# Performance work log

Measured on AMD Instinct MI355X. Metric: run time of the kernel, lower is better.

Reference implementation:

```python
import jax, jax.numpy as jnp
import numpy as np
import math

N = 8192
F_IN = 1024
F_OUT = 1024
MAX_ITER = 10


def whale_optimizer(positions, key, max_iter=MAX_ITER):
    """Vectorized whale optimization algorithm.

    Faithful to the original per-agent/per-dim update rules, but the agent
    loop is vectorized (on-device RNG, one parallel update per outer
    iteration); only the `max_iter` outer iterations stay sequential.
    positions: [N, D] float32.
    """
    n, d = positions.shape
    lower = jnp.min(positions)
    upper = jnp.max(positions)
    k0, loop_key = jax.random.split(key)
    leader = positions[jax.random.randint(k0, (), 0, n)]  # [D]

    def step(carry, it):
        pos, leader = carry
        itf = it.astype(jnp.float32)
        k = jax.random.fold_in(loop_key, it)
        k1, k2, k3, k4, k5, k6 = jax.random.split(k, 6)
        a = 2.0 - itf * (2.0 / max_iter)
        a2 = -1.0 + itf * (-1.0 / max_iter)
        r1 = jax.random.uniform(k1, (n, 1))
        r2 = jax.random.uniform(k2, (n, 1))
        A = 2.0 * a * r1 - a                       # [n,1]
        C = 2.0 * r2                               # [n,1]
        lp = (a2 - 1.0) * jax.random.uniform(k3, (n, 1)) + 1.0  # spiral param
        p = jax.random.uniform(k4, (n, 1))
        # random leader per (agent, dim), as in the original inner j-loop
        ridx = jax.random.randint(k5, (n, d), 0, n)
        x_rand = jnp.take_along_axis(pos, ridx, axis=0)         # [n,d]
        explore = jnp.abs(x_rand - A * jnp.abs(C * x_rand - pos))
        exploit = jnp.abs(leader - A * jnp.abs(C * leader - pos))
        spiral = jnp.abs(jnp.abs(leader - pos) * jnp.exp(lp) * jnp.cos(2.0 * jnp.pi * lp) + leader)
        new_pos = jnp.where(p < 0.5,
                            jnp.where(jnp.abs(A) >= 1.0, explore, exploit),
                            spiral)
        new_pos = jnp.clip(new_pos, lower, upper)
        new_leader = new_pos[jax.random.randint(k6, (), 0, n)]
        return (new_pos, new_leader), None

    (positions, _), _ = jax.lax.scan(step, (positions, leader), jnp.arange(max_iter))
    return positions


def setup_inputs() -> dict:
    key = jax.random.key(0)
    k1, k2, k3, k4 = jax.random.split(key, 4)
    stdv = 1.0 / math.sqrt(F_OUT)
    return {
        "input": jax.random.normal(k1, (N, F_IN), dtype=jnp.float32),
        "adj": jax.random.uniform(k2, (N, N), dtype=jnp.float32) * (1.0 / N),
        "h0": jax.random.normal(k3, (N, F_IN), dtype=jnp.float32),
        "weight": jax.random.uniform(k4, (F_IN, F_OUT), dtype=jnp.float32,
                                      minval=-stdv, maxval=stdv),
        "lamda": jnp.float32(0.5),
        "alpha": jnp.float32(0.1),
        "l": 1,
    }


def reference(input, adj, h0, weight, lamda, alpha, l):
    # variant=False, residual=False
    theta = jnp.log(lamda / l + 1.0)
    hi = adj @ input                                  # spmm(adj, input)
    support = (1.0 - alpha) * hi + alpha * h0
    r = support
    # original detaches support before the whale optimizer
    opt = whale_optimizer(jax.lax.stop_gradient(support), jax.random.key(42))
    output = theta * (opt @ weight) + (1.0 - theta) * r
    return output
```

## Files before the change

kernel.cpp:

```cpp
#include <hip/hip_runtime.h>
#include <hip/hip_bf16.h>
#include <stdint.h>
#include <math.h>

typedef uint32_t u32;
typedef __hip_bfloat16 bf16t;
typedef __attribute__((ext_vector_type(8))) short short8;
typedef __attribute__((ext_vector_type(4))) float f32x4;


__host__ __device__ __forceinline__ void tf2(u32 k0, u32 k1, u32 c0, u32 c1, u32& o0, u32& o1) {
  const u32 ks2 = k0 ^ k1 ^ 0x1BD11BDAu;
  u32 x0 = c0 + k0, x1 = c1 + k1;
#define TFROT(v,r) (((v)<<(r))|((v)>>(32-(r))))
#define TFR(r) { x0 += x1; x1 = TFROT(x1,r); x1 ^= x0; }
  TFR(13) TFR(15) TFR(26) TFR(6)   x0 += k1;  x1 += ks2 + 1u;
  TFR(17) TFR(29) TFR(16) TFR(24)  x0 += ks2; x1 += k0 + 2u;
  TFR(13) TFR(15) TFR(26) TFR(6)   x0 += k0;  x1 += k1 + 3u;
  TFR(17) TFR(29) TFR(16) TFR(24)  x0 += k1;  x1 += ks2 + 4u;
  TFR(13) TFR(15) TFR(26) TFR(6)   x0 += ks2; x1 += k0 + 5u;
#undef TFR
#undef TFROT
  o0 = x0; o1 = x1;
}

__device__ __forceinline__ float unif_row(u32 ka, u32 kb, int i) {
  u32 o0, o1;
  tf2(ka, kb, 0u, (u32)i, o0, o1);
  return __uint_as_float(0x3F800000u | ((o0 ^ o1) >> 9)) - 1.0f;
}

__device__ __forceinline__ int ridx_fn(u32 ka, u32 kb, u32 f) {
  u32 o0, o1; tf2(ka, kb, 0u, f, o0, o1); return (int)((o0 ^ o1) & 8191u);
}

static inline void split2(u32 ka, u32 kb, u32* kA, u32* kB) {
  u32 a0, a1, b0, b1;
  tf2(ka, kb, 0u, 0u, a0, a1);
  tf2(ka, kb, 0u, 1u, b0, b1);
  kA[0] = a0; kA[1] = a1; kB[0] = b0; kB[1] = b1;
}

static inline void split6(u32 ka, u32 kb, u32 out[6][2]) {
  for (u32 i = 0; i < 6; i++) { u32 o0, o1; tf2(ka, kb, 0u, i, o0, o1); out[i][0] = o0; out[i][1] = o1; }
}

static inline int scalar_randint8192(u32 ka, u32 kb) {
  u32 kA[2], kB[2];
  split2(ka, kb, kA, kB);
  u32 o0, o1;
  tf2(kB[0], kB[1], 0u, 0u, o0, o1);
  return (int)((o0 ^ o1) & 8191u);
}

__device__ __forceinline__ ushort f2bf(float f) {
  u32 u = __float_as_uint(f);
  u32 r = u + 0x7FFFu + ((u >> 16) & 1u);
  return (ushort)(r >> 16);
}

__device__ __forceinline__ void packa_body(int idx, const float* __restrict__ A, uint4* __restrict__ out,
                                           int K, int lgS) {
  const int S = K >> 6;
  const int chunk = idx >> 10;
  const int w = idx & 1023;
  const int r = w >> 3, kq = w & 7;
  const int cm = chunk >> lgS, s = chunk & (S - 1);
  const float* src = A + (size_t)((cm << 7) + r) * K + (s << 6) + (kq << 3);
  const float4 f0 = *(const float4*)src;
  const float4 f1 = *(const float4*)(src + 4);
  u32 wv[4];
  wv[0] = (u32)f2bf(f0.x) | ((u32)f2bf(f0.y) << 16);
  wv[1] = (u32)f2bf(f0.z) | ((u32)f2bf(f0.w) << 16);
  wv[2] = (u32)f2bf(f1.x) | ((u32)f2bf(f1.y) << 16);
  wv[3] = (u32)f2bf(f1.z) | ((u32)f2bf(f1.w) << 16);
  uint4 o; o.x = wv[0]; o.y = wv[1]; o.z = wv[2]; o.w = wv[3];
  out[((size_t)chunk << 10) + (r << 3) + (kq ^ (r & 7))] = o;
}

__device__ __forceinline__ void packb_body(int idx, const float* __restrict__ B, uint4* __restrict__ out,
                                           int Nn) {
  const int g = idx / Nn;
  const int n = idx - g * Nn;
  u32 wv[4];
#pragma unroll
  for (int j = 0; j < 4; j++) {
    const float f0 = B[(size_t)(g * 8 + 2 * j) * Nn + n];
    const float f1 = B[(size_t)(g * 8 + 2 * j + 1) * Nn + n];
    wv[j] = (u32)f2bf(f0) | ((u32)f2bf(f1) << 16);
  }
  uint4 o; o.x = wv[0]; o.y = wv[1]; o.z = wv[2]; o.w = wv[3];
  out[idx] = o;
}

__global__ __launch_bounds__(256) void pack_all_k(
    const float* __restrict__ adj, uint4* __restrict__ apk,
    const float* __restrict__ inp, uint4* __restrict__ b1p,
    const float* __restrict__ wgt, uint4* __restrict__ wp) {
  const int b = blockIdx.x;
  const int tid = threadIdx.x;
  if (b < 32768) {
    packa_body(b * 256 + tid, adj, apk, 8192, 7);
  } else if (b < 36864) {
    packb_body((b - 32768) * 256 + tid, inp, b1p, 1024);
  } else {
    packb_body((b - 36864) * 256 + tid, wgt, wp, 1024);
  }
}

__global__ __launch_bounds__(256) void minmax2_k(const float* __restrict__ part, int G, float* __restrict__ bnd) {
  __shared__ float slo[256], shi[256];
  const int tid = threadIdx.x;
  float lo = 3.4e38f, hi = -3.4e38f;
  for (int i = tid; i < G; i += 256) { lo = fminf(lo, part[i]); hi = fmaxf(hi, part[G + i]); }
  slo[tid] = lo; shi[tid] = hi; __syncthreads();
  for (int s = 128; s > 0; s >>= 1) {
    if (tid < s) { slo[tid] = fminf(slo[tid], slo[tid + s]); shi[tid] = fmaxf(shi[tid], shi[tid + s]); }
    __syncthreads();
  }
  if (tid == 0) { bnd[0] = slo[0]; bnd[1] = shi[0]; }
}

__device__ __forceinline__ void gld_lds16(const void* g, void* l) {
  __builtin_amdgcn_global_load_lds((const __attribute__((address_space(1))) void*)g,
                                   (__attribute__((address_space(3))) void*)l, 16, 0, 0);
}

template <int EPI>
__global__ __launch_bounds__(256, 2) void gemm_k(
    const bf16t* __restrict__ Ap, const bf16t* __restrict__ Bp,
    const float* __restrict__ aux, const float* __restrict__ sF,
    const int* __restrict__ sI, float* __restrict__ C,
    float* __restrict__ prt, int PG, int Nn, int K) {
  __shared__ __align__(16) bf16t As[2][8192];
  __shared__ __align__(16) bf16t Bs[2][8192];
  const int tid = threadIdx.x;
  const int lane = tid & 63;
  const int wave = tid >> 6;
  const int bm = blockIdx.x & 63;
  const int bn = blockIdx.x >> 6;
  const int m0 = bm << 7, n0 = bn << 7;
  const int wm = (wave & 1) << 6;
  const int wn = (wave >> 1) << 6;
  const int S = K >> 6;

  f32x4 acc[4][4];
#pragma unroll
  for (int i = 0; i < 4; i++)
#pragma unroll
    for (int j = 0; j < 4; j++) acc[i][j] = (f32x4){0.f, 0.f, 0.f, 0.f};

  const bf16t* gA0 = Ap + (((size_t)bm * S) << 13);
  const bf16t* gBj[4];
  const size_t bstep = (size_t)Nn * 64;
#pragma unroll
  for (int j = 0; j < 4; j++) {
    const int u = tid + (j << 8);
    gBj[j] = Bp + ((size_t)(u >> 7) * Nn + n0 + (u & 127)) * 8;
  }
  auto stage = [&](int s, int buf) {
    const bf16t* a = gA0 + ((size_t)s << 13);
#pragma unroll
    for (int j = 0; j < 4; j++) {
      const int u = tid + (j << 8);
      gld_lds16(a + ((size_t)u << 3), &As[buf][u << 3]);
    }
#pragma unroll
    for (int j = 0; j < 4; j++) {
      const int u = tid + (j << 8);
      gld_lds16(gBj[j] + (size_t)s * bstep, &Bs[buf][u << 3]);
    }
  };

  const int arow = lane & 15, aq = lane >> 4;
  const int abase = ((wm + arow) << 6) + ((aq ^ (arow & 7)) << 3);
  const int bbase = ((aq << 7) + wn + arow) << 3;

  stage(0, 0);

  for (int s = 0; s < S; ++s) {
    const int cur = s & 1;
    __syncthreads();
    if (s + 1 < S) stage(s + 1, cur ^ 1);
#pragma unroll
    for (int c = 0; c < 2; ++c) {
      short8 af[4], bv[4];
      const int ab = abase ^ (c << 5);
#pragma unroll
      for (int mt = 0; mt < 4; mt++)
        af[mt] = *(const short8*)(&As[cur][ab + mt * 1024]);
#pragma unroll
      for (int nt = 0; nt < 4; nt++)
        bv[nt] = *(const short8*)(&Bs[cur][bbase + (c << 12) + (nt << 7)]);
#pragma unroll
      for (int mt = 0; mt < 4; mt++)
#pragma unroll
        for (int nt = 0; nt < 4; nt++)
          acc[mt][nt] = __builtin_amdgcn_mfma_f32_16x16x32_bf16(af[mt], bv[nt], acc[mt][nt], 0, 0, 0);
    }
  }

  float p1, p2;
  if (EPI == 1) { const float al = sF[0]; p1 = 1.0f - al; p2 = al; }
  else { const float th = logf(sF[0] / (float)sI[0] + 1.0f); p1 = th; p2 = 1.0f - th; }
  const int col = lane & 15, rq = lane >> 4;
  float vlo = 3.4e38f, vhi = -3.4e38f;
#pragma unroll
  for (int mt = 0; mt < 4; mt++)
#pragma unroll
    for (int nt = 0; nt < 4; nt++)
#pragma unroll
      for (int r = 0; r < 4; r++) {
        const int gm = m0 + wm + mt * 16 + (rq << 2) + r;
        const int gn = n0 + wn + nt * 16 + col;
        const size_t ix = (size_t)gm * Nn + gn;
        const float v = p1 * acc[mt][nt][r] + p2 * aux[ix];
        C[ix] = v;
        if (EPI == 1) { vlo = fminf(vlo, v); vhi = fmaxf(vhi, v); }
      }
  if (EPI == 1) {
    __syncthreads();
    float* red = (float*)&As[0][0];
    red[tid] = vlo; red[256 + tid] = vhi;
    __syncthreads();
    for (int s = 128; s > 0; s >>= 1) {
      if (tid < s) {
        red[tid] = fminf(red[tid], red[tid + s]);
        red[256 + tid] = fmaxf(red[256 + tid], red[256 + tid + s]);
      }
      __syncthreads();
    }
    if (tid == 0) { prt[blockIdx.x] = red[0]; prt[PG + blockIdx.x] = red[256]; }
  }
}

struct WA {
  u32 k1a, k1b, k2a, k2b, k3a, k3b, k4a, k4b, k5a, k5b;
  int ldr;
  float a, a2;
};

__global__ __launch_bounds__(256) void whale_k(
    const float* __restrict__ pinb, float* __restrict__ poutb,
    ushort* __restrict__ opt, const float* __restrict__ bnd, WA w) {
  const int tid = threadIdx.x;
  const int wave = tid >> 6, lane = tid & 63;
  const int row = (blockIdx.x << 2) + wave;
  const float lo = bnd[0], hi = bnd[1];
  const float r1 = unif_row(w.k1a, w.k1b, row);
  const float r2 = unif_row(w.k2a, w.k2b, row);
  const float u3 = unif_row(w.k3a, w.k3b, row);
  const float p  = unif_row(w.k4a, w.k4b, row);
  float t2 = (2.0f * w.a) * r1;
  asm volatile("" : "+v"(t2));
  const float A = t2 - w.a;
  const float Cc = 2.0f * r2;
  const float* pin = pinb + ((size_t)row << 10);
  float4 pv[4];
#pragma unroll
  for (int k = 0; k < 4; ++k) pv[k] = *(const float4*)(pin + ((lane + (k << 6)) << 2));

  float ov[4][4];
  const bool bp = (p < 0.5f);
  const bool ex = bp && (fabsf(A) >= 1.0f);
  if (ex) {
    int ri[4][4];
#pragma unroll
    for (int k = 0; k < 4; ++k) {
      const u32 fb = ((u32)row << 10) + (u32)((lane + (k << 6)) << 2);
#pragma unroll
      for (int e = 0; e < 4; ++e) ri[k][e] = ridx_fn(w.k5a, w.k5b, fb + (u32)e);
    }
    float xr[4][4];
#pragma unroll
    for (int k = 0; k < 4; ++k) {
      const int j0 = (lane + (k << 6)) << 2;
#pragma unroll
      for (int e = 0; e < 4; ++e) xr[k][e] = pinb[((size_t)ri[k][e] << 10) + j0 + e];
    }
#pragma unroll
    for (int k = 0; k < 4; ++k)
#pragma unroll
      for (int e = 0; e < 4; ++e) {
        const float pos = (&pv[k].x)[e];
        ov[k][e] = fabsf(xr[k][e] - A * fabsf(Cc * xr[k][e] - pos));
      }
  } else {
    const float* ldp = pinb + ((size_t)w.ldr << 10);
    float4 lv[4];
#pragma unroll
    for (int k = 0; k < 4; ++k) lv[k] = *(const float4*)(ldp + ((lane + (k << 6)) << 2));
    if (bp) {
#pragma unroll
      for (int k = 0; k < 4; ++k)
#pragma unroll
        for (int e = 0; e < 4; ++e) {
          const float pos = (&pv[k].x)[e], ld = (&lv[k].x)[e];
          ov[k][e] = fabsf(ld - A * fabsf(Cc * ld - pos));
        }
    } else {
      const float lp = (w.a2 - 1.0f) * u3 + 1.0f;
      const float s1 = expf(lp);
      const float s2 = cosf(6.2831855f * lp);
#pragma unroll
      for (int k = 0; k < 4; ++k)
#pragma unroll
        for (int e = 0; e < 4; ++e) {
          const float pos = (&pv[k].x)[e], ld = (&lv[k].x)[e];
          ov[k][e] = fabsf(fabsf(ld - pos) * s1 * s2 + ld);
        }
    }
  }
#pragma unroll
  for (int k = 0; k < 4; ++k) {
    const int j0 = (lane + (k << 6)) << 2;
    float4 res;
#pragma unroll
    for (int e = 0; e < 4; ++e) (&res.x)[e] = fminf(fmaxf(ov[k][e], lo), hi);
    if (!opt) {
      *(float4*)(poutb + ((size_t)row << 10) + j0) = res;
    } else {
      ushort4 o4;
      o4.x = f2bf(res.x); o4.y = f2bf(res.y); o4.z = f2bf(res.z); o4.w = f2bf(res.w);
      const int rw = row & 127;
      const size_t chunk = (size_t)((row >> 7) << 4) + (j0 >> 6);
      ushort* dst = opt + (chunk << 13) + (rw << 6) + ((((j0 >> 3) & 7) ^ (rw & 7)) << 3) + (j0 & 7);
      *(ushort4*)dst = o4;
    }
  }
}

extern "C" void kernel_launch(void* const* d_in, const int* in_sizes, int n_in,
                              void* d_out, int out_size, void* d_ws, size_t ws_size,
                              hipStream_t stream) {
  const float* inp = (const float*)d_in[0];
  const float* adj = (const float*)d_in[1];
  const float* h0  = (const float*)d_in[2];
  const float* wgt = (const float*)d_in[3];
  const float* lam = (const float*)d_in[4];
  const float* alp = (const float*)d_in[5];
  const int* lint  = (const int*)d_in[6];

  float* outp = (float*)d_out;

  char* ws = (char*)d_ws;
  bf16t* Apk  = (bf16t*)(ws);
  float* P0   = (float*)(ws);
  float* P1   = (float*)(ws + 33554432);
  ushort* OPT = (ushort*)(ws + 67108864);
  bf16t* B1p  = (bf16t*)(ws + 134217728);
  bf16t* Wp   = (bf16t*)(ws + 150994944);
  float* SUP  = (float*)(ws + 153092096);
  float* PRT  = (float*)(ws + 186646528);
  float* BND  = (float*)(ws + 186662912);

  hipLaunchKernelGGL(pack_all_k, dim3(37376), dim3(256), 0, stream,
                     adj, (uint4*)Apk, inp, (uint4*)B1p, wgt, (uint4*)Wp);
  hipLaunchKernelGGL((gemm_k<1>), dim3(512), dim3(256), 0, stream, Apk, B1p, h0, alp, lint,
                     SUP, PRT, 512, 1024, 8192);
  hipLaunchKernelGGL(minmax2_k, dim3(1), dim3(256), 0, stream, PRT, 512, BND);

  u32 k0k[2], lpk[2];
  split2(0u, 42u, k0k, lpk);
  int ldr = scalar_randint8192(k0k[0], k0k[1]);
  const float* cur = SUP;
  float* bufs[2] = {P0, P1};
  for (int it = 0; it < 10; ++it) {
    u32 ka, kb; tf2(lpk[0], lpk[1], 0u, (u32)it, ka, kb);
    u32 ks[6][2];
    split6(ka, kb, ks);
    u32 k5A[2], k5B[2];
    split2(ks[4][0], ks[4][1], k5A, k5B);
    WA w;
    w.k1a = ks[0][0]; w.k1b = ks[0][1];
    w.k2a = ks[1][0]; w.k2b = ks[1][1];
    w.k3a = ks[2][0]; w.k3b = ks[2][1];
    w.k4a = ks[3][0]; w.k4b = ks[3][1];
    w.k5a = k5B[0];   w.k5b = k5B[1];
    w.ldr = ldr;
    const float itf = (float)it;
    w.a = 2.0f - itf * 0.2f;
    w.a2 = -1.0f + itf * (-0.1f);
    float* nxt = bufs[it & 1];
    hipLaunchKernelGGL(whale_k, dim3(2048), dim3(256), 0, stream, cur, nxt,
                       (it == 9) ? OPT : (ushort*)nullptr, BND, w);
    cur = nxt;
    ldr = scalar_randint8192(ks[5][0], ks[5][1]);
  }
  hipLaunchKernelGGL((gemm_k<2>), dim3(512), dim3(256), 0, stream, (const bf16t*)OPT, Wp, SUP, lam, lint,
                     outp, (float*)nullptr, 0, 1024, 1024);
  (void)in_sizes; (void)n_in; (void)out_size; (void)ws_size;
}
```

Measured before the change: 869.8 us.

## Fuse last five whale iterations into one kernel with precomputed leader chain

For iterations 5-9, where |A|<1 guarantees no explore branch and hence no random gather, the leader rows are propagated by a small single-block kernel and then each row applies five updates in registers in one fused kernel. The host checks that no r1 hits zero so |A|<1 holds for every row, and falls back to per-iteration kernels otherwise. This removes four full read/write passes over the 32MB position array and several launches, at the cost of a serial host scan over 8192 Threefry evaluations.

```diff
diff --git a/kernel.cpp b/kernel.cpp
--- a/kernel.cpp
+++ b/kernel.cpp
@@ -24,7 +24,7 @@
   o0 = x0; o1 = x1;
 }
 
-__device__ __forceinline__ float unif_row(u32 ka, u32 kb, int i) {
+__host__ __device__ __forceinline__ float unif_row(u32 ka, u32 kb, int i) {
   u32 o0, o1;
   tf2(ka, kb, 0u, (u32)i, o0, o1);
   return __uint_as_float(0x3F800000u | ((o0 ^ o1) >> 9)) - 1.0f;
@@ -53,7 +53,7 @@
   return (int)((o0 ^ o1) & 8191u);
 }
 
-__device__ __forceinline__ ushort f2bf(float f) {
+__host__ __device__ __forceinline__ ushort f2bf(float f) {
   u32 u = __float_as_uint(f);
   u32 r = u + 0x7FFFu + ((u >> 16) & 1u);
   return (ushort)(r >> 16);
@@ -239,6 +239,8 @@
   int ldr;
   float a, a2;
 };
+struct WP { u32 k1a, k1b, k2a, k2b, k3a, k3b, k4a, k4b; float a, a2; int ldr; };
+struct F5 { WP w[5]; };
 
 __global__ __launch_bounds__(256) void whale_k(
     const float* __restrict__ pinb, float* __restrict__ poutb,
@@ -330,6 +332,85 @@
   }
 }
 
+template <int NK>
+__device__ __forceinline__ void upd_row(const WP w, int row, float lo, float hi,
+                                        const float4* lv, float4* x) {
+  const float r1 = unif_row(w.k1a, w.k1b, row);
+  const float r2 = unif_row(w.k2a, w.k2b, row);
+  const float u3 = unif_row(w.k3a, w.k3b, row);
+  const float p  = unif_row(w.k4a, w.k4b, row);
+  float t2 = (2.0f * w.a) * r1;
+  asm volatile("" : "+v"(t2));
+  const float A = t2 - w.a;
+  const float Cc = 2.0f * r2;
+  const bool bp = (p < 0.5f);
+  float s1 = 0.f, s2 = 0.f;
+  if (!bp) {
+    const float lp = (w.a2 - 1.0f) * u3 + 1.0f;
+    s1 = expf(lp);
+    s2 = cosf(6.2831855f * lp);
+  }
+#pragma unroll
+  for (int k = 0; k < NK; ++k)
+#pragma unroll
+    for (int e = 0; e < 4; ++e) {
+      const float pos = (&x[k].x)[e], ld = (&lv[k].x)[e];
+      const float ov = bp ? fabsf(ld - A * fabsf(Cc * ld - pos))
+                          : fabsf(fabsf(ld - pos) * s1 * s2 + ld);
+      (&x[k].x)[e] = fminf(fmaxf(ov, lo), hi);
+    }
+}
+
+__global__ __launch_bounds__(256) void ldrchain_k(
+    const float* __restrict__ p4, const float* __restrict__ bnd,
+    float* __restrict__ V, F5 f) {
+  const int j0 = threadIdx.x << 2;
+  const float lo = bnd[0], hi = bnd[1];
+  float4 v[5];
+  v[0] = *(const float4*)(p4 + ((size_t)f.w[0].ldr << 10) + j0);
+  *(float4*)(V + j0) = v[0];
+#pragma unroll
+  for (int t = 1; t < 5; ++t) {
+    const int row = f.w[t].ldr;
+    float4 x = *(const float4*)(p4 + ((size_t)row << 10) + j0);
+#pragma unroll
+    for (int q = 0; q < t; ++q) upd_row<1>(f.w[q], row, lo, hi, &v[q], &x);
+    v[t] = x;
+    *(float4*)(V + (t << 10) + j0) = x;
+  }
+}
+
+__global__ __launch_bounds__(256) void fused5_k(
+    const float* __restrict__ p4, const float* __restrict__ V,
+    const float* __restrict__ bnd, ushort* __restrict__ opt, F5 f) {
+  const int tid = threadIdx.x;
+  const int wave = tid >> 6, lane = tid & 63;
+  const int row = (blockIdx.x << 2) + wave;
+  const float lo = bnd[0], hi = bnd[1];
+  const float* pin = p4 + ((size_t)row << 10);
+  float4 x[4];
+#pragma unroll
+  for (int k = 0; k < 4; ++k) x[k] = *(const float4*)(pin + ((lane + (k << 6)) << 2));
+#pragma unroll
+  for (int it = 0; it < 5; ++it) {
+    float4 lv[4];
+#pragma unroll
+    for (int k = 0; k < 4; ++k)
+      lv[k] = *(const float4*)(V + (it << 10) + ((lane + (k << 6)) << 2));
+    upd_row<4>(f.w[it], row, lo, hi, lv, x);
+  }
+#pragma unroll
+  for (int k = 0; k < 4; ++k) {
+    const int j0 = (lane + (k << 6)) << 2;
+    ushort4 o4;
+    o4.x = f2bf(x[k].x); o4.y = f2bf(x[k].y); o4.z = f2bf(x[k].z); o4.w = f2bf(x[k].w);
+    const int rw = row & 127;
+    const size_t chunk = (size_t)((row >> 7) << 4) + (j0 >> 6);
+    ushort* dst = opt + (chunk << 13) + (rw << 6) + ((((j0 >> 3) & 7) ^ (rw & 7)) << 3) + (j0 & 7);
+    *(ushort4*)dst = o4;
+  }
+}
+
 extern "C" void kernel_launch(void* const* d_in, const int* in_sizes, int n_in,
                               void* d_out, int out_size, void* d_ws, size_t ws_size,
                               hipStream_t stream) {
@@ -353,6 +434,7 @@
   float* SUP  = (float*)(ws + 153092096);
   float* PRT  = (float*)(ws + 186646528);
   float* BND  = (float*)(ws + 186662912);
+  float* LDRV = (float*)(ws + 186663168);
 
   hipLaunchKernelGGL(pack_all_k, dim3(37376), dim3(256), 0, stream,
                      adj, (uint4*)Apk, inp, (uint4*)B1p, wgt, (uint4*)Wp);
@@ -363,15 +445,14 @@
   u32 k0k[2], lpk[2];
   split2(0u, 42u, k0k, lpk);
   int ldr = scalar_randint8192(k0k[0], k0k[1]);
-  const float* cur = SUP;
-  float* bufs[2] = {P0, P1};
+  WA wa[10];
   for (int it = 0; it < 10; ++it) {
     u32 ka, kb; tf2(lpk[0], lpk[1], 0u, (u32)it, ka, kb);
     u32 ks[6][2];
     split6(ka, kb, ks);
     u32 k5A[2], k5B[2];
     split2(ks[4][0], ks[4][1], k5A, k5B);
-    WA w;
+    WA& w = wa[it];
     w.k1a = ks[0][0]; w.k1b = ks[0][1];
     w.k2a = ks[1][0]; w.k2b = ks[1][1];
     w.k3a = ks[2][0]; w.k3b = ks[2][1];
@@ -381,11 +462,41 @@
     const float itf = (float)it;
     w.a = 2.0f - itf * 0.2f;
     w.a2 = -1.0f + itf * (-0.1f);
+    ldr = scalar_randint8192(ks[5][0], ks[5][1]);
+  }
+  bool safe5 = true;
+  for (int r = 0; r < 8192 && safe5; ++r) {
+    u32 o0, o1; tf2(wa[5].k1a, wa[5].k1b, 0u, (u32)r, o0, o1);
+    if (((o0 ^ o1) >> 9) == 0u) safe5 = false;
+  }
+
+  const float* cur = SUP;
+  float* bufs[2] = {P0, P1};
+  for (int it = 0; it < 5; ++it) {
     float* nxt = bufs[it & 1];
     hipLaunchKernelGGL(whale_k, dim3(2048), dim3(256), 0, stream, cur, nxt,
-                       (it == 9) ? OPT : (ushort*)nullptr, BND, w);
+                       (ushort*)nullptr, BND, wa[it]);
     cur = nxt;
-    ldr = scalar_randint8192(ks[5][0], ks[5][1]);
+  }
+  if (safe5) {
+    F5 f;
+    for (int t = 0; t < 5; ++t) {
+      const WA& w = wa[5 + t];
+      f.w[t].k1a = w.k1a; f.w[t].k1b = w.k1b;
+      f.w[t].k2a = w.k2a; f.w[t].k2b = w.k2b;
+      f.w[t].k3a = w.k3a; f.w[t].k3b = w.k3b;
+      f.w[t].k4a = w.k4a; f.w[t].k4b = w.k4b;
+      f.w[t].a = w.a; f.w[t].a2 = w.a2; f.w[t].ldr = w.ldr;
+    }
+    hipLaunchKernelGGL(ldrchain_k, dim3(1), dim3(256), 0, stream, cur, BND, LDRV, f);
+    hipLaunchKernelGGL(fused5_k, dim3(2048), dim3(256), 0, stream, cur, LDRV, BND, OPT, f);
+  } else {
+    for (int it = 5; it < 10; ++it) {
+      float* nxt = bufs[it & 1];
+      hipLaunchKernelGGL(whale_k, dim3(2048), dim3(256), 0, stream, cur, nxt,
+                         (it == 9) ? OPT : (ushort*)nullptr, BND, wa[it]);
+      cur = nxt;
+    }
   }
   hipLaunchKernelGGL((gemm_k<2>), dim3(512), dim3(256), 0, stream, (const bf16t*)OPT, Wp, SUP, lam, lint,
                      outp, (float*)nullptr, 0, 1024, 1024);
```

Measured after the change: 857.0 us. No clear change (-1.5%).
